# Kernel tuning notes

Hardware: AMD Instinct MI355X
Metric: run time of the kernel (lower is better)

## Reference

```python
import jax, jax.numpy as jnp
import numpy as np

B, T, C = 16, 64, 512


def setup_inputs() -> dict:
    key = jax.random.key(0)
    ks = jax.random.split(key, 12)
    s = 1.0 / np.sqrt(C)
    st = 1.0 / np.sqrt(2.0)
    return {
        "x": jax.random.normal(ks[0], (B, T, C), dtype=jnp.float32),
        "ts": jax.random.uniform(ks[1], (B, T), dtype=jnp.float32),
        "attn_mask": jnp.ones((B, T), dtype=jnp.float32),
        # project: Linear(C, C)
        "W_proj": jax.random.uniform(ks[2], (C, C), jnp.float32, -s, s),
        "b_proj": jax.random.uniform(ks[3], (C,), jnp.float32, -s, s),
        # embed_xs: Linear(C, C)
        "W_x": jax.random.uniform(ks[4], (C, C), jnp.float32, -s, s),
        "b_x": jax.random.uniform(ks[5], (C,), jnp.float32, -s, s),
        # embed_ts: Linear(2, C)
        "W_t": jax.random.uniform(ks[6], (2, C), jnp.float32, -st, st),
        "b_t": jax.random.uniform(ks[7], (C,), jnp.float32, -st, st),
        # get_importances Linear(C, C)
        "W_imp": jax.random.uniform(ks[8], (C, C), jnp.float32, -s, s),
        "b_imp": jax.random.uniform(ks[9], (C,), jnp.float32, -s, s),
    }


def reference(x, ts, attn_mask, W_proj, b_proj, W_x, b_x, W_t, b_t, W_imp, b_imp):
    # x: [B,T,C], ts: [B,T], attn_mask: [B,T]
    values = (x @ W_proj + b_proj)[:, None, :, :]          # [B,1,T,C]
    rel = ts[:, :, None] - ts[:, None, :]                  # [B,T,T]
    rel2 = jnp.log1p(jnp.maximum(jnp.stack([rel, -rel], axis=-1), 0.0))  # [B,T,T,2]
    h = rel2 @ W_t + b_t                                   # [B,T,T,C] (include_t)
    h = h + (x @ W_x + b_x)[:, None, :, :]                 # include_x, broadcast over dim 1
    importances = jax.nn.sigmoid(jax.nn.relu(h) @ W_imp + b_imp)  # [B,T,T,C]
    importances = importances * attn_mask[:, None, :, None]
    interactions = jax.nn.logsumexp(values * importances, axis=2)  # [B,T,C]
    return (x + interactions, importances.mean(axis=3))
```

## Files before the change

kernel.cpp:

```cpp
#include <hip/hip_runtime.h>
#include <hip/hip_bf16.h>

#define Bn 16
#define Tn 64
#define Cn 512
#define LDA  520
#define LDA8 528

#define LOG2E 1.4426950408889634f
#define LN2   0.6931471805599453f
#define ASC 16.0f
#define WSC 256.0f
#define ZSC (1.0f/4096.0f)

typedef short s8v __attribute__((ext_vector_type(8)));
typedef float f4v __attribute__((ext_vector_type(4)));
typedef unsigned long ul2 __attribute__((ext_vector_type(2)));

__device__ __forceinline__ unsigned int pk2bf(float a, float b){
  __hip_bfloat162 t = __float22bfloat162_rn(make_float2(a, b));
  union { __hip_bfloat162 h; unsigned int u; } c; c.h = t; return c.u;
}
__device__ __forceinline__ float bits2f(unsigned int u){
  union { unsigned int u; float f; } c; c.u = u; return c.f;
}

__global__ void swz(const float* __restrict__ Wp, const float* __restrict__ Wx,
                    const float* __restrict__ Wi, const float* __restrict__ ts,
                    unsigned short* __restrict__ WswB, unsigned char* __restrict__ Wsw8,
                    float* __restrict__ R){
  int blk = blockIdx.x;
  if(blk < 256){
    int gid = blk * 256 + threadIdx.x;
    int mat = gid >> 15, rem = gid & 32767;
    int lane = rem & 63, st = rem >> 6, t = st & 31, s = st >> 5;
    int n  = t * 16 + (lane & 15);
    int k0 = s * 32 + ((lane >> 4) << 3);
    const float* W = mat ? Wx : Wp;
    unsigned int p[4];
#pragma unroll
    for(int q = 0; q < 4; ++q)
      p[q] = pk2bf(W[(k0 + 2*q) * Cn + n], W[(k0 + 2*q + 1) * Cn + n]);
    uint4 o; o.x = p[0]; o.y = p[1]; o.z = p[2]; o.w = p[3];
    *reinterpret_cast<uint4*>(WswB + (size_t)mat * 262144 + (size_t)rem * 8) = o;
  } else if(blk < 384){
    int rem = (blk - 256) * 256 + threadIdx.x;
    int nt = rem & 3, lane = (rem >> 2) & 63, w8 = (rem >> 8) & 7, s = rem >> 11;
    int n  = (w8 * 4 + nt) * 16 + (lane & 15);
    int k0 = s * 32 + ((lane >> 4) << 3);
    float v[8];
#pragma unroll
    for(int j = 0; j < 8; ++j) v[j] = Wi[(k0 + j) * Cn + n] * WSC;
    int d0 = __builtin_amdgcn_cvt_pk_fp8_f32(v[0], v[1], 0, false);
    d0     = __builtin_amdgcn_cvt_pk_fp8_f32(v[2], v[3], d0, true);
    int d1 = __builtin_amdgcn_cvt_pk_fp8_f32(v[4], v[5], 0, false);
    d1     = __builtin_amdgcn_cvt_pk_fp8_f32(v[6], v[7], d1, true);
    uint2 o; o.x = (unsigned int)d0; o.y = (unsigned int)d1;
    *reinterpret_cast<uint2*>(Wsw8 + (size_t)((s * 8 + w8) * 64 + lane) * 32 + nt * 8) = o;
  } else {
    int gid2 = (blk - 384) * 256 + threadIdx.x;
    float r[8];
#pragma unroll
    for(int q = 0; q < 4; ++q){
      int p = gid2 * 4 + q;
      int b = p >> 12, i = (p >> 6) & 63, j = p & 63;
      float d = ts[b * Tn + i] - ts[b * Tn + j];
      r[2*q]   = __logf(1.f + fmaxf(d, 0.f));
      r[2*q+1] = __logf(1.f + fmaxf(-d, 0.f));
    }
    float4* Rf4 = reinterpret_cast<float4*>(R);
    Rf4[gid2 * 2    ] = make_float4(r[0], r[1], r[2], r[3]);
    Rf4[gid2 * 2 + 1] = make_float4(r[4], r[5], r[6], r[7]);
  }
}

__global__ __launch_bounds__(256)
void prep(const float* __restrict__ x, const float* __restrict__ bp,
          const float* __restrict__ bx, const float* __restrict__ bt,
          const unsigned short* __restrict__ WswB,
          float* __restrict__ xe, unsigned short* __restrict__ vfrag){
  __shared__ unsigned short lA[Tn * LDA];
  const int blk = blockIdx.x;
  const int b = blk >> 4, mat = (blk >> 3) & 1, oct = blk & 7;
  const int tid = threadIdx.x;
  const int lane = tid & 63, w2 = tid >> 6, quad = lane >> 4, ln = lane & 15;
  const int t = oct * 4 + w2;

  const s8v* Bp = reinterpret_cast<const s8v*>(WswB + (size_t)mat * 262144) + (t * 64 + lane);
  s8v bcur = Bp[0];

  const int c0 = (tid & 127) * 4, jb = tid >> 7;
#pragma unroll
  for(int it = 0; it < 32; ++it){
    int j = jb + it * 2;
    f4v xv = *reinterpret_cast<const f4v*>(x + ((b * Tn + j) * Cn + c0));
    uint2 uu; uu.x = pk2bf(xv[0], xv[1]); uu.y = pk2bf(xv[2], xv[3]);
    *reinterpret_cast<uint2*>(&lA[j * LDA + c0]) = uu;
  }
  __syncthreads();

  s8v a[4], an[4];
#pragma unroll
  for(int mt = 0; mt < 4; ++mt)
    a[mt] = *reinterpret_cast<const s8v*>(&lA[(mt * 16 + ln) * LDA + quad * 8]);
  f4v acc[4];
#pragma unroll
  for(int mt = 0; mt < 4; ++mt){ acc[mt][0]=0.f; acc[mt][1]=0.f; acc[mt][2]=0.f; acc[mt][3]=0.f; }

#pragma unroll 2
  for(int s = 0; s < 16; ++s){
    int sn = (s + 1) & 15;
    s8v bn = Bp[sn * 2048];
#pragma unroll
    for(int mt = 0; mt < 4; ++mt)
      an[mt] = *reinterpret_cast<const s8v*>(&lA[(mt * 16 + ln) * LDA + sn * 32 + quad * 8]);
#pragma unroll
    for(int mt = 0; mt < 4; ++mt)
      acc[mt] = __builtin_amdgcn_mfma_f32_16x16x32_bf16(a[mt], bcur, acc[mt], 0, 0, 0);
#pragma unroll
    for(int mt = 0; mt < 4; ++mt) a[mt] = an[mt];
    bcur = bn;
  }

  const int c = t * 16 + ln;
  if(mat == 0){
    float bb = bp[c];
    const int eb_h = w2 & 1;
#pragma unroll
    for(int mt = 0; mt < 4; ++mt){
      float v0 = (acc[mt][0] + bb) * LOG2E;
      float v1 = (acc[mt][1] + bb) * LOG2E;
      float v2 = (acc[mt][2] + bb) * LOG2E;
      float v3 = (acc[mt][3] + bb) * LOG2E;
      uint2 o; o.x = pk2bf(v0, v1); o.y = pk2bf(v2, v3);
      int eb = mt * 2 + (w2 >> 1);
      *reinterpret_cast<uint2*>(vfrag + ((size_t)((b * 8 + oct) * 8 + eb) * 64 + lane) * 8 + eb_h * 4) = o;
    }
  } else {
    float bb = bx[c] + bt[c];
#pragma unroll
    for(int mt = 0; mt < 4; ++mt)
#pragma unroll
      for(int r = 0; r < 4; ++r){
        int j = mt * 16 + quad * 4 + r;
        xe[(b * Tn + j) * Cn + c] = (acc[mt][r] + bb) * ASC;
      }
  }
}

__global__ __launch_bounds__(512, 4)
void fused(const float* __restrict__ x, const float* __restrict__ am,
           const float* __restrict__ Wt, const float* __restrict__ bimp,
           const unsigned char* __restrict__ Wsw8, const float* __restrict__ R,
           const float* __restrict__ xe, const unsigned short* __restrict__ vfrag,
           float* __restrict__ out0, float* __restrict__ out1){
  __shared__ unsigned char lA8[Tn * LDA8];
  __shared__ float msk[Tn], rr0[Tn], rr1[Tn], rsum[Tn];
  const int b = blockIdx.x >> 6, i = blockIdx.x & 63;
  const int tid = threadIdx.x;
  if(tid < Tn){
    msk[tid] = am[b * Tn + tid];
    rsum[tid] = 0.f;
    float2 rv = reinterpret_cast<const float2*>(R)[(b * Tn + i) * Tn + tid];
    rr0[tid] = rv.x; rr1[tid] = rv.y;
  }
  __syncthreads();

  const int lane = tid & 63, w = tid >> 6, quad = lane >> 4, ln = lane & 15;
  const ul2* Bv = reinterpret_cast<const ul2*>(Wsw8);
  const int off = (w * 64 + lane) * 2;
  ul2 b01 = Bv[off], b23 = Bv[off + 1];

  const int c0 = (tid & 127) * 4, jb = tid >> 7;
  f4v wt0 = *reinterpret_cast<const f4v*>(Wt + c0);
  f4v wt1 = *reinterpret_cast<const f4v*>(Wt + Cn + c0);
  wt0[0]*=ASC; wt0[1]*=ASC; wt0[2]*=ASC; wt0[3]*=ASC;
  wt1[0]*=ASC; wt1[1]*=ASC; wt1[2]*=ASC; wt1[3]*=ASC;
#pragma unroll
  for(int it = 0; it < 16; ++it){
    int j = jb + it * 4;
    float r0 = rr0[j], r1 = rr1[j];
    f4v xv = *reinterpret_cast<const f4v*>(xe + ((b * Tn + j) * Cn + c0));
    float h0 = fmaxf(fmaf(r1, wt1[0], fmaf(r0, wt0[0], xv[0])), 0.f);
    float h1 = fmaxf(fmaf(r1, wt1[1], fmaf(r0, wt0[1], xv[1])), 0.f);
    float h2 = fmaxf(fmaf(r1, wt1[2], fmaf(r0, wt0[2], xv[2])), 0.f);
    float h3 = fmaxf(fmaf(r1, wt1[3], fmaf(r0, wt0[3], xv[3])), 0.f);
    int d = __builtin_amdgcn_cvt_pk_fp8_f32(h0, h1, 0, false);
    d     = __builtin_amdgcn_cvt_pk_fp8_f32(h2, h3, d, true);
    *reinterpret_cast<int*>(lA8 + j * LDA8 + c0) = d;
  }
  __syncthreads();

  unsigned long a[4], an[4];
#pragma unroll
  for(int mt = 0; mt < 4; ++mt)
    a[mt] = *reinterpret_cast<const unsigned long*>(lA8 + (mt * 16 + ln) * LDA8 + quad * 8);
  f4v acc[4][4];
#pragma unroll
  for(int mt = 0; mt < 4; ++mt)
#pragma unroll
    for(int nt = 0; nt < 4; ++nt){
      acc[mt][nt][0]=0.f; acc[mt][nt][1]=0.f; acc[mt][nt][2]=0.f; acc[mt][nt][3]=0.f;
    }

#pragma unroll 2
  for(int s = 0; s < 16; ++s){
    int sn = (s + 1) & 15;
    ul2 nb01 = Bv[sn * 1024 + off];
    ul2 nb23 = Bv[sn * 1024 + off + 1];
#pragma unroll
    for(int mt = 0; mt < 4; ++mt)
      an[mt] = *reinterpret_cast<const unsigned long*>(lA8 + (mt * 16 + ln) * LDA8 + sn * 32 + quad * 8);
    long bf0 = (long)b01.x, bf1 = (long)b01.y, bf2 = (long)b23.x, bf3 = (long)b23.y;
#pragma unroll
    for(int mt = 0; mt < 4; ++mt){
      acc[mt][0] = __builtin_amdgcn_mfma_f32_16x16x32_fp8_fp8((long)a[mt], bf0, acc[mt][0], 0, 0, 0);
      acc[mt][1] = __builtin_amdgcn_mfma_f32_16x16x32_fp8_fp8((long)a[mt], bf1, acc[mt][1], 0, 0, 0);
      acc[mt][2] = __builtin_amdgcn_mfma_f32_16x16x32_fp8_fp8((long)a[mt], bf2, acc[mt][2], 0, 0, 0);
      acc[mt][3] = __builtin_amdgcn_mfma_f32_16x16x32_fp8_fp8((long)a[mt], bf3, acc[mt][3], 0, 0, 0);
    }
#pragma unroll
    for(int mt = 0; mt < 4; ++mt) a[mt] = an[mt];
    b01 = nb01; b23 = nb23;
  }

  uint4 vv[8];
#pragma unroll
  for(int eb = 0; eb < 8; ++eb)
    vv[eb] = *reinterpret_cast<const uint4*>(vfrag + ((size_t)((b * 8 + w) * 8 + eb) * 64 + lane) * 8);

  float bb[4];
#pragma unroll
  for(int nt = 0; nt < 4; ++nt) bb[nt] = bimp[w * 64 + nt * 16 + ln];
#pragma unroll
  for(int mt = 0; mt < 4; ++mt)
#pragma unroll
    for(int r = 0; r < 4; ++r){
      float mk = msk[mt * 16 + quad * 4 + r];
      float p = 0.f;
#pragma unroll
      for(int nt = 0; nt < 4; ++nt){
        float z = fmaf(acc[mt][nt][r], ZSC, bb[nt]);
        float im = mk * __builtin_amdgcn_rcpf(1.f + __builtin_amdgcn_exp2f(z * -LOG2E));
        acc[mt][nt][r] = im;
        p += im;
      }
      p += __shfl_xor(p, 1, 64);
      p += __shfl_xor(p, 2, 64);
      p += __shfl_xor(p, 4, 64);
      p += __shfl_xor(p, 8, 64);
      if(ln == 0) atomicAdd(&rsum[mt * 16 + quad * 4 + r], p);
    }
  __syncthreads();
  if(tid < Tn) out1[(b * Tn + i) * Tn + tid] = rsum[tid] * (1.f / 512.f);

  const unsigned int* vw = reinterpret_cast<const unsigned int*>(vv);
#pragma unroll
  for(int nt = 0; nt < 4; ++nt){
    float se = 0.f;
#pragma unroll
    for(int mt = 0; mt < 4; ++mt)
#pragma unroll
      for(int r = 0; r < 4; ++r){
        int e = mt * 16 + nt * 4 + r;
        unsigned int d = vw[e >> 1];
        float vl = bits2f((e & 1) ? (d & 0xffff0000u) : (d << 16));
        se += __builtin_amdgcn_exp2f(vl * acc[mt][nt][r]);
      }
    se += __shfl_xor(se, 16, 64);
    se += __shfl_xor(se, 32, 64);
    if(quad == 0){
      int idx = (b * Tn + i) * Cn + (w * 64 + nt * 16 + ln);
      out0[idx] = x[idx] + __builtin_amdgcn_logf(se) * LN2;
    }
  }
}

extern "C" void kernel_launch(void* const* d_in, const int* in_sizes, int n_in,
                              void* d_out, int out_size, void* d_ws, size_t ws_size,
                              hipStream_t stream){
  const float* x    = (const float*)d_in[0];
  const float* ts   = (const float*)d_in[1];
  const float* am   = (const float*)d_in[2];
  const float* Wp   = (const float*)d_in[3];
  const float* bp   = (const float*)d_in[4];
  const float* Wx   = (const float*)d_in[5];
  const float* bx   = (const float*)d_in[6];
  const float* Wt   = (const float*)d_in[7];
  const float* bt   = (const float*)d_in[8];
  const float* Wi   = (const float*)d_in[9];
  const float* bimp = (const float*)d_in[10];
  float* out0 = (float*)d_out;
  float* out1 = out0 + Bn * Tn * Cn;

  char* ws = (char*)d_ws;
  unsigned short* WswB  = (unsigned short*)ws;
  unsigned char*  Wsw8  = (unsigned char*)(ws + 1048576);
  float*          xe    = (float*)(ws + 1310720);
  unsigned short* vfrag = (unsigned short*)(ws + 3407872);
  float*          R     = (float*)(ws + 4456448);

  swz<<<448, 256, 0, stream>>>(Wp, Wx, Wi, ts, WswB, Wsw8, R);
  prep<<<256, 256, 0, stream>>>(x, bp, bx, bt, WswB, xe, vfrag);
  fused<<<1024, 512, 0, stream>>>(x, am, Wt, bimp, Wsw8, R, xe, vfrag, out0, out1);
}
```

Baseline: 126.3 us.

## Merge swizzle and prep kernels, load projection weights directly, stagger fused K-loop

The separate bf16 weight-swizzle kernel is removed. The projection GEMM now loads fp32 W_proj/W_x directly from global memory and packs them to bf16 in registers, which lets the R table, fp8 W_imp swizzle and projection work share one launch and drops a kernel boundary and an intermediate buffer. In the fused kernel, the xe loads are hoisted ahead of the first barrier. The K-loop start is also offset by block parity, with a two-deep B-fragment prefetch, so neighbouring blocks read different weight slices. The cost is strided uncoalesced fp32 weight loads in the projection blocks, and more register pressure from 16 preloaded float4s.

```diff
diff --git a/kernel.cpp b/kernel.cpp
--- a/kernel.cpp
+++ b/kernel.cpp
@@ -24,27 +24,41 @@
 __device__ __forceinline__ float bits2f(unsigned int u){
   union { unsigned int u; float f; } c; c.u = u; return c.f;
 }
-
-__global__ void swz(const float* __restrict__ Wp, const float* __restrict__ Wx,
-                    const float* __restrict__ Wi, const float* __restrict__ ts,
-                    unsigned short* __restrict__ WswB, unsigned char* __restrict__ Wsw8,
-                    float* __restrict__ R){
-  int blk = blockIdx.x;
-  if(blk < 256){
-    int gid = blk * 256 + threadIdx.x;
-    int mat = gid >> 15, rem = gid & 32767;
-    int lane = rem & 63, st = rem >> 6, t = st & 31, s = st >> 5;
-    int n  = t * 16 + (lane & 15);
-    int k0 = s * 32 + ((lane >> 4) << 3);
-    const float* W = mat ? Wx : Wp;
-    unsigned int p[4];
-#pragma unroll
-    for(int q = 0; q < 4; ++q)
-      p[q] = pk2bf(W[(k0 + 2*q) * Cn + n], W[(k0 + 2*q + 1) * Cn + n]);
-    uint4 o; o.x = p[0]; o.y = p[1]; o.z = p[2]; o.w = p[3];
-    *reinterpret_cast<uint4*>(WswB + (size_t)mat * 262144 + (size_t)rem * 8) = o;
-  } else if(blk < 384){
-    int rem = (blk - 256) * 256 + threadIdx.x;
+__device__ __forceinline__ s8v pack_bf8(const float* v){
+  union { uint4 u; s8v s; } c;
+  c.u.x = pk2bf(v[0], v[1]); c.u.y = pk2bf(v[2], v[3]);
+  c.u.z = pk2bf(v[4], v[5]); c.u.w = pk2bf(v[6], v[7]);
+  return c.s;
+}
+
+__global__ __launch_bounds__(256)
+void pre(const float* __restrict__ x, const float* __restrict__ ts,
+         const float* __restrict__ Wp, const float* __restrict__ bp,
+         const float* __restrict__ Wx, const float* __restrict__ bx,
+         const float* __restrict__ bt, const float* __restrict__ Wi,
+         float* __restrict__ xe, unsigned short* __restrict__ vfrag,
+         unsigned char* __restrict__ Wsw8, float* __restrict__ R){
+  __shared__ unsigned short lA[Tn * LDA];
+  const int blk = blockIdx.x;
+  const int tid = threadIdx.x;
+  if(blk < 64){
+    int gid2 = blk * 256 + tid;
+    float r[8];
+#pragma unroll
+    for(int q = 0; q < 4; ++q){
+      int p = gid2 * 4 + q;
+      int b = p >> 12, i = (p >> 6) & 63, j = p & 63;
+      float d = ts[b * Tn + i] - ts[b * Tn + j];
+      r[2*q]   = __logf(1.f + fmaxf(d, 0.f));
+      r[2*q+1] = __logf(1.f + fmaxf(-d, 0.f));
+    }
+    float4* Rf4 = reinterpret_cast<float4*>(R);
+    Rf4[gid2 * 2    ] = make_float4(r[0], r[1], r[2], r[3]);
+    Rf4[gid2 * 2 + 1] = make_float4(r[4], r[5], r[6], r[7]);
+    return;
+  }
+  if(blk < 192){
+    int rem = (blk - 64) * 256 + tid;
     int nt = rem & 3, lane = (rem >> 2) & 63, w8 = (rem >> 8) & 7, s = rem >> 11;
     int n  = (w8 * 4 + nt) * 16 + (lane & 15);
     int k0 = s * 32 + ((lane >> 4) << 3);
@@ -57,37 +71,14 @@
     d1     = __builtin_amdgcn_cvt_pk_fp8_f32(v[6], v[7], d1, true);
     uint2 o; o.x = (unsigned int)d0; o.y = (unsigned int)d1;
     *reinterpret_cast<uint2*>(Wsw8 + (size_t)((s * 8 + w8) * 64 + lane) * 32 + nt * 8) = o;
-  } else {
-    int gid2 = (blk - 384) * 256 + threadIdx.x;
-    float r[8];
-#pragma unroll
-    for(int q = 0; q < 4; ++q){
-      int p = gid2 * 4 + q;
-      int b = p >> 12, i = (p >> 6) & 63, j = p & 63;
-      float d = ts[b * Tn + i] - ts[b * Tn + j];
-      r[2*q]   = __logf(1.f + fmaxf(d, 0.f));
-      r[2*q+1] = __logf(1.f + fmaxf(-d, 0.f));
-    }
-    float4* Rf4 = reinterpret_cast<float4*>(R);
-    Rf4[gid2 * 2    ] = make_float4(r[0], r[1], r[2], r[3]);
-    Rf4[gid2 * 2 + 1] = make_float4(r[4], r[5], r[6], r[7]);
-  }
-}
-
-__global__ __launch_bounds__(256)
-void prep(const float* __restrict__ x, const float* __restrict__ bp,
-          const float* __restrict__ bx, const float* __restrict__ bt,
-          const unsigned short* __restrict__ WswB,
-          float* __restrict__ xe, unsigned short* __restrict__ vfrag){
-  __shared__ unsigned short lA[Tn * LDA];
-  const int blk = blockIdx.x;
-  const int b = blk >> 4, mat = (blk >> 3) & 1, oct = blk & 7;
-  const int tid = threadIdx.x;
+    return;
+  }
+  const int idx = blk - 192;
+  const int b = idx >> 4, mat = (idx >> 3) & 1, oct = idx & 7;
   const int lane = tid & 63, w2 = tid >> 6, quad = lane >> 4, ln = lane & 15;
   const int t = oct * 4 + w2;
-
-  const s8v* Bp = reinterpret_cast<const s8v*>(WswB + (size_t)mat * 262144) + (t * 64 + lane);
-  s8v bcur = Bp[0];
+  const float* Wg = mat ? Wx : Wp;
+  const float* wb = Wg + (size_t)(quad * 8) * Cn + t * 16 + ln;
 
   const int c0 = (tid & 127) * 4, jb = tid >> 7;
 #pragma unroll
@@ -97,6 +88,9 @@
     uint2 uu; uu.x = pk2bf(xv[0], xv[1]); uu.y = pk2bf(xv[2], xv[3]);
     *reinterpret_cast<uint2*>(&lA[j * LDA + c0]) = uu;
   }
+  float wv[8];
+#pragma unroll
+  for(int j = 0; j < 8; ++j) wv[j] = wb[j * Cn];
   __syncthreads();
 
   s8v a[4], an[4];
@@ -106,11 +100,14 @@
   f4v acc[4];
 #pragma unroll
   for(int mt = 0; mt < 4; ++mt){ acc[mt][0]=0.f; acc[mt][1]=0.f; acc[mt][2]=0.f; acc[mt][3]=0.f; }
+  s8v bcur = pack_bf8(wv);
 
 #pragma unroll 2
   for(int s = 0; s < 16; ++s){
     int sn = (s + 1) & 15;
-    s8v bn = Bp[sn * 2048];
+    float wn[8];
+#pragma unroll
+    for(int j = 0; j < 8; ++j) wn[j] = wb[(size_t)sn * 32 * Cn + j * Cn];
 #pragma unroll
     for(int mt = 0; mt < 4; ++mt)
       an[mt] = *reinterpret_cast<const s8v*>(&lA[(mt * 16 + ln) * LDA + sn * 32 + quad * 8]);
@@ -119,7 +116,7 @@
       acc[mt] = __builtin_amdgcn_mfma_f32_16x16x32_bf16(a[mt], bcur, acc[mt], 0, 0, 0);
 #pragma unroll
     for(int mt = 0; mt < 4; ++mt) a[mt] = an[mt];
-    bcur = bn;
+    bcur = pack_bf8(wn);
   }
 
   const int c = t * 16 + ln;
@@ -158,20 +155,30 @@
   __shared__ float msk[Tn], rr0[Tn], rr1[Tn], rsum[Tn];
   const int b = blockIdx.x >> 6, i = blockIdx.x & 63;
   const int tid = threadIdx.x;
+  const int lane = tid & 63, w = tid >> 6, quad = lane >> 4, ln = lane & 15;
+  const int ph = (blockIdx.x & 1) << 3;
+
+  float mv = 0.f; float2 rv = make_float2(0.f, 0.f);
   if(tid < Tn){
-    msk[tid] = am[b * Tn + tid];
-    rsum[tid] = 0.f;
-    float2 rv = reinterpret_cast<const float2*>(R)[(b * Tn + i) * Tn + tid];
-    rr0[tid] = rv.x; rr1[tid] = rv.y;
-  }
-  __syncthreads();
-
-  const int lane = tid & 63, w = tid >> 6, quad = lane >> 4, ln = lane & 15;
+    mv = am[b * Tn + tid];
+    rv = reinterpret_cast<const float2*>(R)[(b * Tn + i) * Tn + tid];
+  }
+
+  const int c0 = (tid & 127) * 4, jb = tid >> 7;
+  f4v xv[16];
+#pragma unroll
+  for(int it = 0; it < 16; ++it)
+    xv[it] = *reinterpret_cast<const f4v*>(xe + ((b * Tn + (jb + it * 4)) * Cn + c0));
+
   const ul2* Bv = reinterpret_cast<const ul2*>(Wsw8);
   const int off = (w * 64 + lane) * 2;
-  ul2 b01 = Bv[off], b23 = Bv[off + 1];
-
-  const int c0 = (tid & 127) * 4, jb = tid >> 7;
+  ul2 bA[2], bB[2];
+  bA[0] = Bv[ph * 1024 + off];       bB[0] = Bv[ph * 1024 + off + 1];
+  bA[1] = Bv[(ph + 1) * 1024 + off]; bB[1] = Bv[(ph + 1) * 1024 + off + 1];
+
+  if(tid < Tn){ msk[tid] = mv; rr0[tid] = rv.x; rr1[tid] = rv.y; rsum[tid] = 0.f; }
+  __syncthreads();
+
   f4v wt0 = *reinterpret_cast<const f4v*>(Wt + c0);
   f4v wt1 = *reinterpret_cast<const f4v*>(Wt + Cn + c0);
   wt0[0]*=ASC; wt0[1]*=ASC; wt0[2]*=ASC; wt0[3]*=ASC;
@@ -180,11 +187,10 @@
   for(int it = 0; it < 16; ++it){
     int j = jb + it * 4;
     float r0 = rr0[j], r1 = rr1[j];
-    f4v xv = *reinterpret_cast<const f4v*>(xe + ((b * Tn + j) * Cn + c0));
-    float h0 = fmaxf(fmaf(r1, wt1[0], fmaf(r0, wt0[0], xv[0])), 0.f);
-    float h1 = fmaxf(fmaf(r1, wt1[1], fmaf(r0, wt0[1], xv[1])), 0.f);
-    float h2 = fmaxf(fmaf(r1, wt1[2], fmaf(r0, wt0[2], xv[2])), 0.f);
-    float h3 = fmaxf(fmaf(r1, wt1[3], fmaf(r0, wt0[3], xv[3])), 0.f);
+    float h0 = fmaxf(fmaf(r1, wt1[0], fmaf(r0, wt0[0], xv[it][0])), 0.f);
+    float h1 = fmaxf(fmaf(r1, wt1[1], fmaf(r0, wt0[1], xv[it][1])), 0.f);
+    float h2 = fmaxf(fmaf(r1, wt1[2], fmaf(r0, wt0[2], xv[it][2])), 0.f);
+    float h3 = fmaxf(fmaf(r1, wt1[3], fmaf(r0, wt0[3], xv[it][3])), 0.f);
     int d = __builtin_amdgcn_cvt_pk_fp8_f32(h0, h1, 0, false);
     d     = __builtin_amdgcn_cvt_pk_fp8_f32(h2, h3, d, true);
     *reinterpret_cast<int*>(lA8 + j * LDA8 + c0) = d;
@@ -194,7 +200,7 @@
   unsigned long a[4], an[4];
 #pragma unroll
   for(int mt = 0; mt < 4; ++mt)
-    a[mt] = *reinterpret_cast<const unsigned long*>(lA8 + (mt * 16 + ln) * LDA8 + quad * 8);
+    a[mt] = *reinterpret_cast<const unsigned long*>(lA8 + (mt * 16 + ln) * LDA8 + ph * 32 + quad * 8);
   f4v acc[4][4];
 #pragma unroll
   for(int mt = 0; mt < 4; ++mt)
@@ -205,13 +211,16 @@
 
 #pragma unroll 2
   for(int s = 0; s < 16; ++s){
-    int sn = (s + 1) & 15;
-    ul2 nb01 = Bv[sn * 1024 + off];
-    ul2 nb23 = Bv[sn * 1024 + off + 1];
-#pragma unroll
-    for(int mt = 0; mt < 4; ++mt)
-      an[mt] = *reinterpret_cast<const unsigned long*>(lA8 + (mt * 16 + ln) * LDA8 + sn * 32 + quad * 8);
-    long bf0 = (long)b01.x, bf1 = (long)b01.y, bf2 = (long)b23.x, bf3 = (long)b23.y;
+    const int sc = s & 1;
+    const int p2 = (s + 2 + ph) & 15;
+    const int p1 = (s + 1 + ph) & 15;
+    ul2 nb0 = Bv[p2 * 1024 + off];
+    ul2 nb1 = Bv[p2 * 1024 + off + 1];
+#pragma unroll
+    for(int mt = 0; mt < 4; ++mt)
+      an[mt] = *reinterpret_cast<const unsigned long*>(lA8 + (mt * 16 + ln) * LDA8 + p1 * 32 + quad * 8);
+    long bf0 = (long)bA[sc].x, bf1 = (long)bA[sc].y;
+    long bf2 = (long)bB[sc].x, bf3 = (long)bB[sc].y;
 #pragma unroll
     for(int mt = 0; mt < 4; ++mt){
       acc[mt][0] = __builtin_amdgcn_mfma_f32_16x16x32_fp8_fp8((long)a[mt], bf0, acc[mt][0], 0, 0, 0);
@@ -221,7 +230,7 @@
     }
 #pragma unroll
     for(int mt = 0; mt < 4; ++mt) a[mt] = an[mt];
-    b01 = nb01; b23 = nb23;
+    bA[sc] = nb0; bB[sc] = nb1;
   }
 
   uint4 vv[8];
@@ -294,13 +303,11 @@
   float* out1 = out0 + Bn * Tn * Cn;
 
   char* ws = (char*)d_ws;
-  unsigned short* WswB  = (unsigned short*)ws;
-  unsigned char*  Wsw8  = (unsigned char*)(ws + 1048576);
-  float*          xe    = (float*)(ws + 1310720);
-  unsigned short* vfrag = (unsigned short*)(ws + 3407872);
-  float*          R     = (float*)(ws + 4456448);
-
-  swz<<<448, 256, 0, stream>>>(Wp, Wx, Wi, ts, WswB, Wsw8, R);
-  prep<<<256, 256, 0, stream>>>(x, bp, bx, bt, WswB, xe, vfrag);
+  unsigned char*  Wsw8  = (unsigned char*)ws;
+  float*          xe    = (float*)(ws + 262144);
+  unsigned short* vfrag = (unsigned short*)(ws + 2359296);
+  float*          R     = (float*)(ws + 3407872);
+
+  pre<<<448, 256, 0, stream>>>(x, ts, Wp, bp, Wx, bx, bt, Wi, xe, vfrag, Wsw8, R);
   fused<<<1024, 512, 0, stream>>>(x, am, Wt, bimp, Wsw8, R, xe, vfrag, out0, out1);
 }
```

New measurement: 123.2 us. -2.4%, faster.
